# Optimization experiments

Measured on AMD Instinct MI355X. Metric: run time of the kernel, lower is better.

## Reference

```python
import jax, jax.numpy as jnp
import numpy as np
import math

B, SEQ, H, HKV, D = 2, 2048, 32, 8, 128
BLOCK, LOCAL_BLOCKS, VERT_STRIDE = 64, 16, 8
NB = SEQ // BLOCK


def _build_layout():
    # local + vertical-strided causal block-sparse layout (homo heads),
    # converted from CSR to a padded [NB, max_nnz] column-index table.
    q_idx = np.arange(NB)[:, None]
    k_idx = np.arange(NB)[None, :]
    dense = (k_idx <= q_idx) & ((q_idx - k_idx < LOCAL_BLOCKS) | ((k_idx + 1) % VERT_STRIDE == 0))
    max_nnz = int(dense.sum(1).max())  # == 18 for NB=32, local=16, stride=8
    cols = np.zeros((NB, max_nnz), np.int32)
    valid = np.zeros((NB, max_nnz), np.bool_)
    for i in range(NB):
        c = np.nonzero(dense[i])[0]
        cols[i, :c.size] = c
        valid[i, :c.size] = True
    return jnp.asarray(cols), jnp.asarray(valid)


def setup_inputs() -> dict:
    key = jax.random.key(0)
    kq, kk, kv = jax.random.split(key, 3)
    q = jax.random.normal(kq, (B, SEQ, H, D), jnp.float32)
    k = jax.random.normal(kk, (B, SEQ, HKV, D), jnp.float32)
    v = jax.random.normal(kv, (B, SEQ, HKV, D), jnp.float32)
    layout_cols, layout_mask = _build_layout()
    return {"q": q, "k": k, "v": v, "layout_cols": layout_cols, "layout_mask": layout_mask}


def _attn(q, k, v, layout_cols, layout_mask):
    Bn, S, Hq, Dh = q.shape
    Hkv = k.shape[2]
    g = Hq // Hkv               # GQA group size (q_k_ratio)
    nb, nnz = layout_cols.shape
    blk = S // nb               # block_size
    sm_scale = 1.0 / math.sqrt(Dh)
    # reshape to blocks; keep KV at Hkv heads (no repeat) and group q heads
    qb = q.reshape(Bn, nb, blk, Hkv, g, Dh).transpose(0, 3, 4, 1, 2, 5)  # [B,Hkv,g,nb,blk,D]
    kb = k.reshape(Bn, nb, blk, Hkv, Dh).transpose(0, 3, 1, 2, 4)        # [B,Hkv,nb,blk,D]
    vb = v.reshape(Bn, nb, blk, Hkv, Dh).transpose(0, 3, 1, 2, 4)
    # gather only the attended K/V blocks per query block (honors block sparsity)
    kg = jnp.take(kb, layout_cols, axis=2)  # [B,Hkv,nb,nnz,blk,D]
    vg = jnp.take(vb, layout_cols, axis=2)
    scores = jnp.einsum('bhgqmd,bhqknd->bhgqmkn', qb, kg) * sm_scale  # [B,Hkv,g,nb,blk,nnz,blk]
    # token-level causal mask + padded-column mask (past_len = 0 for prefill)
    q_tok = jnp.arange(nb)[:, None] * blk + jnp.arange(blk)[None, :]            # [nb,blk]
    k_tok = layout_cols[:, :, None] * blk + jnp.arange(blk)[None, None, :]      # [nb,nnz,blk]
    valid = layout_mask[:, None, :, None] & (k_tok[:, None] <= q_tok[:, :, None, None])  # [nb,blk,nnz,blk]
    scores = jnp.where(valid[None, None, None], scores, -jnp.inf)
    p = jax.nn.softmax(scores.reshape(Bn, Hkv, g, nb, blk, nnz * blk), axis=-1).reshape(scores.shape)
    out = jnp.einsum('bhgqmkn,bhqknd->bhgqmd', p, vg)
    return out.transpose(0, 3, 4, 1, 2, 5).reshape(Bn, S, Hq, Dh)


def reference(q, k, v, layout_cols, layout_mask):
    return _attn(q, k, v, layout_cols, layout_mask)
```

## Files before the change

kernel.cpp:

```cpp
#include <hip/hip_runtime.h>

#define B_    2
#define SEQ_  2048
#define H_    32
#define HKV_  8
#define D_    128
#define BLK_  64
#define NB_   32
#define LOCAL_ 16
#define VERT_  8

#define PSTR 72
#define NTASK 512
#define NBLOCK 256

typedef __attribute__((ext_vector_type(8))) short bf16x8;
typedef __attribute__((ext_vector_type(4))) float f32x4;

__device__ __forceinline__ unsigned short f2bf(float f) {
    union { float f; unsigned u; } x; x.f = f;
    unsigned u = x.u;
    return (unsigned short)((u + 0x7FFFu + ((u >> 16) & 1u)) >> 16);
}

__device__ __forceinline__ unsigned pk2(float a, float b) {
#if defined(__has_builtin) && __has_builtin(__builtin_amdgcn_cvt_pk_bf16_f32)
    typedef __attribute__((ext_vector_type(2))) __bf16 bf2;
    bf2 r = __builtin_amdgcn_cvt_pk_bf16_f32(a, b);
    unsigned u; __builtin_memcpy(&u, &r, 4); return u;
#else
    return (unsigned)f2bf(a) | ((unsigned)f2bf(b) << 16);
#endif
}

__device__ __forceinline__ int next_valid(int qb, int j) {
    for (++j; j <= qb; ++j)
        if (((qb - j) < LOCAL_) || (((j + 1) & (VERT_ - 1)) == 0)) return j;
    return qb + 1;
}

__device__ __forceinline__ void dma16(const unsigned short* g, unsigned short* l) {
    __builtin_amdgcn_global_load_lds(
        (const __attribute__((address_space(1))) unsigned int*)g,
        (__attribute__((address_space(3))) unsigned int*)l, 16, 0, 0);
}

__global__ __launch_bounds__(256)
void prepass_kernel(const float* __restrict__ kg, const float* __restrict__ vg,
                    unsigned short* __restrict__ Kws, unsigned short* __restrict__ Vws) {
    __shared__ unsigned short Vt[D_ * 72];
    const int bid = blockIdx.x;
    const int b   = bid >> 8;
    const int hkv = (bid >> 5) & 7;
    const int jb  = bid & 31;
    const int tid = threadIdx.x;
    const int rs  = HKV_ * D_;

    const float* kbase = kg + ((size_t)(b * SEQ_ + jb * BLK_) * HKV_ + hkv) * D_;
    const float* vbase = vg + ((size_t)(b * SEQ_ + jb * BLK_) * HKV_ + hkv) * D_;
    unsigned short* Kdst = Kws + ((size_t)(b * 8 + hkv) * SEQ_ + jb * BLK_) * D_;
    unsigned short* Vdst = Vws + ((size_t)(b * 8 + hkv) * NB_ + jb) * (D_ * BLK_);

#pragma unroll
    for (int t = 0; t < 4; ++t) {
        const int q = t * 256 + tid;
        const int row = q >> 4, c = q & 15;
        const float* p = kbase + (size_t)row * rs + c * 8;
        const float4 a = *(const float4*)p;
        const float4 d4 = *(const float4*)(p + 4);
        uint4 u = { pk2(a.x, a.y), pk2(a.z, a.w), pk2(d4.x, d4.y), pk2(d4.z, d4.w) };
        *(uint4*)&Kdst[row * 128 + ((c ^ (row & 15)) << 3)] = u;
    }
#pragma unroll
    for (int t = 0; t < 8; ++t) {
        const int q = t * 256 + tid;
        const int pos = q >> 5, c4 = q & 31;
        const float4 v4 = *(const float4*)(vbase + (size_t)pos * rs + c4 * 4);
        const unsigned u0 = pk2(v4.x, v4.y), u1 = pk2(v4.z, v4.w);
        Vt[(c4 * 4 + 0) * 72 + pos] = (unsigned short)u0;
        Vt[(c4 * 4 + 1) * 72 + pos] = (unsigned short)(u0 >> 16);
        Vt[(c4 * 4 + 2) * 72 + pos] = (unsigned short)u1;
        Vt[(c4 * 4 + 3) * 72 + pos] = (unsigned short)(u1 >> 16);
    }
    __syncthreads();
#pragma unroll
    for (int t = 0; t < 4; ++t) {
        const int q = t * 256 + tid;
        const int d = q >> 3, c = q & 7;
        const uint2 q0 = *(const uint2*)&Vt[d * 72 + c * 8];
        const uint2 q1 = *(const uint2*)&Vt[d * 72 + c * 8 + 4];
        uint4 u = { q0.x, q0.y, q1.x, q1.y };
        *(uint4*)&Vdst[d * 64 + ((c ^ (d & 7)) << 3)] = u;
    }
}

__global__ __launch_bounds__(1024)
void sparse_attn_v2(const float* __restrict__ qg, float* __restrict__ outg,
                    const unsigned short* __restrict__ Kws,
                    const unsigned short* __restrict__ Vws,
                    unsigned* __restrict__ ctr) {
    __shared__ __align__(16) unsigned short Kb[2][BLK_ * D_];
    __shared__ __align__(16) unsigned short Vb[2][D_ * BLK_];
    __shared__ __align__(16) unsigned short Plds[16 * 16 * PSTR];
    __shared__ unsigned taskLds;

    const int tid  = threadIdx.x;
    const int wave = tid >> 6;
    const int lane = tid & 63;
    const int l15  = lane & 15;
    const int quad = lane >> 4;
    const int hsub = wave >> 2;
    const int rt   = wave & 3;

    int csk[4], csv[2];
#pragma unroll
    for (int s = 0; s < 4; ++s)  csk[s] = ((4 * s + quad) ^ l15) << 3;
#pragma unroll
    for (int s = 0; s < 2; ++s)  csv[s] = ((4 * s + quad) ^ (l15 & 7)) << 3;

    const float c2 = 0.12751649736230723f;
    const short oneb = (short)0x3F80;
    const bf16x8 ones = {oneb, oneb, oneb, oneb, oneb, oneb, oneb, oneb};
    unsigned short* pl = &Plds[wave * 16 * PSTR];

    for (;;) {
        __syncthreads();
        if (tid == 0) taskLds = atomicAdd(ctr, 1u);
        __syncthreads();
        const unsigned t = taskLds;
        if (t >= NTASK) break;

        const int qb  = 31 - (int)(t >> 4);
        const int bh  = (int)(t & 15);
        const int b   = bh >> 3;
        const int hkv = bh & 7;
        const int head = hkv * 4 + hsub;

        const unsigned short* Kbh = Kws + (size_t)(b * 8 + hkv) * SEQ_ * D_;
        const unsigned short* Vbh = Vws + (size_t)(b * 8 + hkv) * NB_ * (D_ * BLK_);

        int j = next_valid(qb, -1);
        dma16(Kbh + (size_t)j * (BLK_ * D_) + tid * 8, &Kb[0][wave * 512]);
        dma16(Vbh + (size_t)j * (D_ * BLK_) + tid * 8, &Vb[0][wave * 512]);

        bf16x8 qf[4];
        {
            const int row = qb * BLK_ + rt * 16 + l15;
            const float* qp = qg + ((size_t)(b * SEQ_ + row) * H_ + head) * D_;
#pragma unroll
            for (int s = 0; s < 4; ++s) {
                const float4 a = *(const float4*)(qp + s * 32 + quad * 8);
                const float4 c = *(const float4*)(qp + s * 32 + quad * 8 + 4);
                uint4 u = { pk2(a.x, a.y), pk2(a.z, a.w), pk2(c.x, c.y), pk2(c.z, c.w) };
                __builtin_memcpy(&qf[s], &u, 16);
            }
        }

        f32x4 lacc = f32x4{0.f, 0.f, 0.f, 0.f};
        f32x4 o_acc[8];
#pragma unroll
        for (int t8 = 0; t8 < 8; ++t8) o_acc[t8] = f32x4{0.f, 0.f, 0.f, 0.f};

        __syncthreads();
        int it = 0;
        while (j <= qb) {
            const int jn = next_valid(qb, j);
            const int cur = it & 1;
            if (jn <= qb) {
                dma16(Kbh + (size_t)jn * (BLK_ * D_) + tid * 8, &Kb[cur ^ 1][wave * 512]);
                dma16(Vbh + (size_t)jn * (D_ * BLK_) + tid * 8, &Vb[cur ^ 1][wave * 512]);
            }

            const unsigned short* kb = Kb[cur];
            f32x4 sacc[4];
#pragma unroll
            for (int t4 = 0; t4 < 4; ++t4) {
                f32x4 acc = f32x4{0.f, 0.f, 0.f, 0.f};
                const unsigned short* krow = kb + (t4 * 16 + l15) * 128;
#pragma unroll
                for (int s = 0; s < 4; ++s) {
                    const bf16x8 kf = *(const bf16x8*)(krow + csk[s]);
                    acc = __builtin_amdgcn_mfma_f32_16x16x32_bf16(qf[s], kf, acc, 0, 0, 0);
                }
                sacc[t4] = acc;
            }

            if (j == qb) {
                const int rowbase = rt * 16 + quad * 4;
#pragma unroll
                for (int t4 = 0; t4 < 4; ++t4) {
                    const int col = t4 * 16 + l15;
#pragma unroll
                    for (int r = 0; r < 4; ++r)
                        if (col > rowbase + r) sacc[t4][r] = -INFINITY;
                }
            }

#pragma unroll
            for (int t4 = 0; t4 < 4; ++t4) {
                const float p0 = exp2f(sacc[t4][0] * c2);
                const float p1 = exp2f(sacc[t4][1] * c2);
                const float p2 = exp2f(sacc[t4][2] * c2);
                const float p3 = exp2f(sacc[t4][3] * c2);
                const unsigned u01 = pk2(p0, p1), u23 = pk2(p2, p3);
                const int cb = t4 * 16 + l15;
                pl[(quad * 4 + 0) * PSTR + cb] = (unsigned short)u01;
                pl[(quad * 4 + 1) * PSTR + cb] = (unsigned short)(u01 >> 16);
                pl[(quad * 4 + 2) * PSTR + cb] = (unsigned short)u23;
                pl[(quad * 4 + 3) * PSTR + cb] = (unsigned short)(u23 >> 16);
            }

            const unsigned short* vb = Vb[cur];
#pragma unroll
            for (int s2 = 0; s2 < 2; ++s2) {
                const bf16x8 pf = *(const bf16x8*)&pl[l15 * PSTR + s2 * 32 + quad * 8];
                lacc = __builtin_amdgcn_mfma_f32_16x16x32_bf16(pf, ones, lacc, 0, 0, 0);
#pragma unroll
                for (int t8 = 0; t8 < 8; ++t8) {
                    const bf16x8 vf = *(const bf16x8*)(vb + (t8 * 16 + l15) * 64 + csv[s2]);
                    o_acc[t8] = __builtin_amdgcn_mfma_f32_16x16x32_bf16(pf, vf, o_acc[t8], 0, 0, 0);
                }
            }

            __syncthreads();
            j = jn; ++it;
        }

        const int orow = qb * BLK_ + rt * 16 + quad * 4;
#pragma unroll
        for (int r = 0; r < 4; ++r) {
            const float inv_l = 1.0f / lacc[r];
            float* op = outg + ((size_t)(b * SEQ_ + orow + r) * H_ + head) * D_;
#pragma unroll
            for (int t8 = 0; t8 < 8; ++t8)
                op[t8 * 16 + l15] = o_acc[t8][r] * inv_l;
        }
    }
}

#define KSTR 136
#define VSTR 72
__global__ __launch_bounds__(1024)
void sparse_attn_v1(const float* __restrict__ qg, const float* __restrict__ kg,
                    const float* __restrict__ vg, float* __restrict__ outg,
                    unsigned* __restrict__ ctr) {
    __shared__ __align__(16) unsigned short Klds[BLK_ * KSTR];
    __shared__ __align__(16) unsigned short Vlds[D_ * VSTR];
    __shared__ __align__(16) unsigned short Plds[16 * 16 * PSTR];
    __shared__ unsigned taskLds;

    const int tid  = threadIdx.x;
    const int wave = tid >> 6;
    const int lane = tid & 63;
    const int l15  = lane & 15;
    const int quad = lane >> 4;
    const int hsub = wave >> 2;
    const int rt   = wave & 3;

    const int srow0 = tid >> 5, srow1 = srow0 + 32;
    const int sc4   = tid & 31;
    const int kld0  = srow0 * KSTR + sc4 * 4, kld1 = srow1 * KSTR + sc4 * 4;
    const int vd    = sc4 * 4;
    const int vskew = (sc4 & 7) << 3;
    const int vp0   = (srow0 + vskew) & 63, vp1 = (srow1 + vskew) & 63;
    const size_t stoff0 = (size_t)srow0 * (HKV_ * D_) + sc4 * 4;
    const size_t stoff1 = (size_t)srow1 * (HKV_ * D_) + sc4 * 4;

    const float c2 = 0.12751649736230723f;
    const short oneb = (short)0x3F80;
    const bf16x8 ones = {oneb, oneb, oneb, oneb, oneb, oneb, oneb, oneb};
    unsigned short* pl = &Plds[wave * 16 * PSTR];

    for (;;) {
        __syncthreads();
        if (tid == 0) taskLds = atomicAdd(ctr, 1u);
        __syncthreads();
        const unsigned t = taskLds;
        if (t >= NTASK) break;
        const int qb  = 31 - (int)(t >> 4);
        const int bh  = (int)(t & 15);
        const int b   = bh >> 3;
        const int hkv = bh & 7;
        const int head = hkv * 4 + hsub;
        const float* kbase = kg + ((size_t)(b * SEQ_) * HKV_ + hkv) * D_;
        const float* vbase = vg + ((size_t)(b * SEQ_) * HKV_ + hkv) * D_;
        bf16x8 qf[4];
        {
            const int row = qb * BLK_ + rt * 16 + l15;
            const float* qp = qg + ((size_t)(b * SEQ_ + row) * H_ + head) * D_;
#pragma unroll
            for (int s = 0; s < 4; ++s) {
                const float4 a = *(const float4*)(qp + s * 32 + quad * 8);
                const float4 c = *(const float4*)(qp + s * 32 + quad * 8 + 4);
                uint4 u = { pk2(a.x, a.y), pk2(a.z, a.w), pk2(c.x, c.y), pk2(c.z, c.w) };
                __builtin_memcpy(&qf[s], &u, 16);
            }
        }
        f32x4 lacc = f32x4{0.f, 0.f, 0.f, 0.f};
        f32x4 o_acc[8];
#pragma unroll
        for (int t8 = 0; t8 < 8; ++t8) o_acc[t8] = f32x4{0.f, 0.f, 0.f, 0.f};
        int j = next_valid(qb, -1);
        float4 kpr0, kpr1, vpr0, vpr1;
        {
            const float* kp = kbase + (size_t)j * BLK_ * HKV_ * D_;
            const float* vp = vbase + (size_t)j * BLK_ * HKV_ * D_;
            kpr0 = *(const float4*)(kp + stoff0); kpr1 = *(const float4*)(kp + stoff1);
            vpr0 = *(const float4*)(vp + stoff0); vpr1 = *(const float4*)(vp + stoff1);
        }
        while (j <= qb) {
            const int jn = next_valid(qb, j);
            __syncthreads();
            {
                uint2 u0 = { pk2(kpr0.x, kpr0.y), pk2(kpr0.z, kpr0.w) };
                uint2 u1 = { pk2(kpr1.x, kpr1.y), pk2(kpr1.z, kpr1.w) };
                *(uint2*)&Klds[kld0] = u0;
                *(uint2*)&Klds[kld1] = u1;
                unsigned a0 = pk2(vpr0.x, vpr0.y), a1 = pk2(vpr0.z, vpr0.w);
                Vlds[(vd + 0) * VSTR + vp0] = (unsigned short)a0;
                Vlds[(vd + 1) * VSTR + vp0] = (unsigned short)(a0 >> 16);
                Vlds[(vd + 2) * VSTR + vp0] = (unsigned short)a1;
                Vlds[(vd + 3) * VSTR + vp0] = (unsigned short)(a1 >> 16);
                unsigned b0 = pk2(vpr1.x, vpr1.y), b1 = pk2(vpr1.z, vpr1.w);
                Vlds[(vd + 0) * VSTR + vp1] = (unsigned short)b0;
                Vlds[(vd + 1) * VSTR + vp1] = (unsigned short)(b0 >> 16);
                Vlds[(vd + 2) * VSTR + vp1] = (unsigned short)b1;
                Vlds[(vd + 3) * VSTR + vp1] = (unsigned short)(b1 >> 16);
            }
            __syncthreads();
            if (jn <= qb) {
                const float* kp = kbase + (size_t)jn * BLK_ * HKV_ * D_;
                const float* vp = vbase + (size_t)jn * BLK_ * HKV_ * D_;
                kpr0 = *(const float4*)(kp + stoff0); kpr1 = *(const float4*)(kp + stoff1);
                vpr0 = *(const float4*)(vp + stoff0); vpr1 = *(const float4*)(vp + stoff1);
            }
            f32x4 sacc[4];
#pragma unroll
            for (int t4 = 0; t4 < 4; ++t4) {
                f32x4 acc = f32x4{0.f, 0.f, 0.f, 0.f};
#pragma unroll
                for (int s = 0; s < 4; ++s) {
                    const bf16x8 kf = *(const bf16x8*)&Klds[(t4 * 16 + l15) * KSTR + s * 32 + quad * 8];
                    acc = __builtin_amdgcn_mfma_f32_16x16x32_bf16(qf[s], kf, acc, 0, 0, 0);
                }
                sacc[t4] = acc;
            }
            if (j == qb) {
                const int rowbase = rt * 16 + quad * 4;
#pragma unroll
                for (int t4 = 0; t4 < 4; ++t4) {
                    const int col = t4 * 16 + l15;
#pragma unroll
                    for (int r = 0; r < 4; ++r)
                        if (col > rowbase + r) sacc[t4][r] = -INFINITY;
                }
            }
#pragma unroll
            for (int t4 = 0; t4 < 4; ++t4) {
                const float p0 = exp2f(sacc[t4][0] * c2);
                const float p1 = exp2f(sacc[t4][1] * c2);
                const float p2 = exp2f(sacc[t4][2] * c2);
                const float p3 = exp2f(sacc[t4][3] * c2);
                const unsigned u01 = pk2(p0, p1), u23 = pk2(p2, p3);
                const int cb = t4 * 16 + l15;
                pl[(quad * 4 + 0) * PSTR + cb] = (unsigned short)u01;
                pl[(quad * 4 + 1) * PSTR + cb] = (unsigned short)(u01 >> 16);
                pl[(quad * 4 + 2) * PSTR + cb] = (unsigned short)u23;
                pl[(quad * 4 + 3) * PSTR + cb] = (unsigned short)(u23 >> 16);
            }
#pragma unroll
            for (int s2 = 0; s2 < 2; ++s2) {
                const bf16x8 pf = *(const bf16x8*)&pl[l15 * PSTR + s2 * 32 + quad * 8];
                lacc = __builtin_amdgcn_mfma_f32_16x16x32_bf16(pf, ones, lacc, 0, 0, 0);
                const int k0 = s2 * 32 + quad * 8;
#pragma unroll
                for (int t8 = 0; t8 < 8; ++t8) {
                    const int n  = t8 * 16 + l15;
                    const int p2 = (k0 + (((n >> 2) & 7) << 3)) & 63;
                    const bf16x8 vf = *(const bf16x8*)&Vlds[n * VSTR + p2];
                    o_acc[t8] = __builtin_amdgcn_mfma_f32_16x16x32_bf16(pf, vf, o_acc[t8], 0, 0, 0);
                }
            }
            j = jn;
        }
        const int orow = qb * BLK_ + rt * 16 + quad * 4;
#pragma unroll
        for (int r = 0; r < 4; ++r) {
            const float inv_l = 1.0f / lacc[r];
            float* op = outg + ((size_t)(b * SEQ_ + orow + r) * H_ + head) * D_;
#pragma unroll
            for (int t8 = 0; t8 < 8; ++t8)
                op[t8 * 16 + l15] = o_acc[t8][r] * inv_l;
        }
    }
}

extern "C" void kernel_launch(void* const* d_in, const int* in_sizes, int n_in,
                              void* d_out, int out_size, void* d_ws, size_t ws_size,
                              hipStream_t stream) {
    const float* q = (const float*)d_in[0];
    const float* k = (const float*)d_in[1];
    const float* v = (const float*)d_in[2];
    float* out = (float*)d_out;

    const size_t kws_elems = (size_t)B_ * HKV_ * SEQ_ * D_;
    const size_t need = 256 + 2 * kws_elems * sizeof(unsigned short);
    if (ws_size >= need) {
        unsigned short* Kws = (unsigned short*)((char*)d_ws + 256);
        unsigned short* Vws = Kws + kws_elems;
        hipMemsetAsync(d_ws, 0, 256, stream);
        prepass_kernel<<<dim3(B_ * HKV_ * NB_), dim3(256), 0, stream>>>(k, v, Kws, Vws);
        sparse_attn_v2<<<dim3(NBLOCK), dim3(1024), 0, stream>>>(q, out, Kws, Vws, (unsigned*)d_ws);
    } else {
        hipMemsetAsync(d_ws, 0, sizeof(unsigned), stream);
        sparse_attn_v1<<<dim3(NBLOCK), dim3(1024), 0, stream>>>(q, k, v, out, (unsigned*)d_ws);
    }
}
```

Baseline: 226.8 us.

## Switch attention kernel to 32x32 MFMA with register-resident P via permlane swap

Rewrites the main sparse attention kernel to use 32x32x16 bf16 MFMA tiles instead of 16x16x32. The S=K·Q^T result is computed transposed so the P matrix can be repacked in registers with permlane32_swap, which removes the LDS round-trip for P. Blocks shrink to 512 threads with two blocks per CU, each wave handling 32 query rows. The upper K half of the diagonal tile is skipped for the first row tile. The cost is more registers per wave from the 16-wide accumulators, and the row/lane mapping is more intricate.

```diff
diff --git a/kernel.cpp b/kernel.cpp
--- a/kernel.cpp
+++ b/kernel.cpp
@@ -16,6 +16,7 @@
 
 typedef __attribute__((ext_vector_type(8))) short bf16x8;
 typedef __attribute__((ext_vector_type(4))) float f32x4;
+typedef __attribute__((ext_vector_type(16))) float f32x16;
 
 __device__ __forceinline__ unsigned short f2bf(float f) {
     union { float f; unsigned u; } x; x.f = f;
@@ -31,6 +32,22 @@
 #else
     return (unsigned)f2bf(a) | ((unsigned)f2bf(b) << 16);
 #endif
+}
+
+__device__ __forceinline__ void pswap(unsigned &a, unsigned &b) {
+#if defined(__has_builtin) && __has_builtin(__builtin_amdgcn_permlane32_swap)
+    auto r = __builtin_amdgcn_permlane32_swap((int)a, (int)b, false, false);
+    a = (unsigned)r[0]; b = (unsigned)r[1];
+#else
+    asm("v_permlane32_swap_b32 %0, %1" : "+v"(a), "+v"(b));
+#endif
+}
+
+__device__ __forceinline__ f32x16 zero16() {
+    f32x16 z;
+#pragma unroll
+    for (int i = 0; i < 16; ++i) z[i] = 0.f;
+    return z;
 }
 
 __device__ __forceinline__ int next_valid(int qb, int j) {
@@ -94,34 +111,33 @@
     }
 }
 
-__global__ __launch_bounds__(1024)
-void sparse_attn_v2(const float* __restrict__ qg, float* __restrict__ outg,
+__global__ __launch_bounds__(512, 2)
+void sparse_attn_v3(const float* __restrict__ qg, float* __restrict__ outg,
                     const unsigned short* __restrict__ Kws,
                     const unsigned short* __restrict__ Vws,
                     unsigned* __restrict__ ctr) {
     __shared__ __align__(16) unsigned short Kb[2][BLK_ * D_];
     __shared__ __align__(16) unsigned short Vb[2][D_ * BLK_];
-    __shared__ __align__(16) unsigned short Plds[16 * 16 * PSTR];
     __shared__ unsigned taskLds;
 
     const int tid  = threadIdx.x;
     const int wave = tid >> 6;
     const int lane = tid & 63;
-    const int l15  = lane & 15;
-    const int quad = lane >> 4;
-    const int hsub = wave >> 2;
-    const int rt   = wave & 3;
-
-    int csk[4], csv[2];
-#pragma unroll
-    for (int s = 0; s < 4; ++s)  csk[s] = ((4 * s + quad) ^ l15) << 3;
-#pragma unroll
-    for (int s = 0; s < 2; ++s)  csv[s] = ((4 * s + quad) ^ (l15 & 7)) << 3;
+    const int q5   = lane & 31;
+    const int h    = lane >> 5;
+    const int hsub = wave >> 1;
+    const int rt2  = wave & 1;
+
+    int cskA[8];
+#pragma unroll
+    for (int dk = 0; dk < 8; ++dk) cskA[dk] = ((((dk * 2) | h) ^ (lane & 15)) << 3);
+    int csvB[4];
+#pragma unroll
+    for (int kc = 0; kc < 4; ++kc) csvB[kc] = ((((kc * 2) | h) ^ (lane & 7)) << 3);
 
     const float c2 = 0.12751649736230723f;
     const short oneb = (short)0x3F80;
     const bf16x8 ones = {oneb, oneb, oneb, oneb, oneb, oneb, oneb, oneb};
-    unsigned short* pl = &Plds[wave * 16 * PSTR];
 
     for (;;) {
         __syncthreads();
@@ -140,26 +156,32 @@
         const unsigned short* Vbh = Vws + (size_t)(b * 8 + hkv) * NB_ * (D_ * BLK_);
 
         int j = next_valid(qb, -1);
-        dma16(Kbh + (size_t)j * (BLK_ * D_) + tid * 8, &Kb[0][wave * 512]);
-        dma16(Vbh + (size_t)j * (D_ * BLK_) + tid * 8, &Vb[0][wave * 512]);
-
-        bf16x8 qf[4];
         {
-            const int row = qb * BLK_ + rt * 16 + l15;
-            const float* qp = qg + ((size_t)(b * SEQ_ + row) * H_ + head) * D_;
-#pragma unroll
-            for (int s = 0; s < 4; ++s) {
-                const float4 a = *(const float4*)(qp + s * 32 + quad * 8);
-                const float4 c = *(const float4*)(qp + s * 32 + quad * 8 + 4);
+            const size_t off = (size_t)j * (BLK_ * D_);
+#pragma unroll
+            for (int i = 0; i < 2; ++i) {
+                dma16(Kbh + off + i * 4096 + tid * 8, &Kb[0][i * 4096 + wave * 512]);
+                dma16(Vbh + off + i * 4096 + tid * 8, &Vb[0][i * 4096 + wave * 512]);
+            }
+        }
+
+        bf16x8 qf[8];
+        {
+            const int row = qb * BLK_ + rt2 * 32 + q5;
+            const float* qp = qg + ((size_t)(b * SEQ_ + row) * H_ + head) * D_ + h * 8;
+#pragma unroll
+            for (int dk = 0; dk < 8; ++dk) {
+                const float4 a = *(const float4*)(qp + dk * 16);
+                const float4 c = *(const float4*)(qp + dk * 16 + 4);
                 uint4 u = { pk2(a.x, a.y), pk2(a.z, a.w), pk2(c.x, c.y), pk2(c.z, c.w) };
-                __builtin_memcpy(&qf[s], &u, 16);
-            }
-        }
-
-        f32x4 lacc = f32x4{0.f, 0.f, 0.f, 0.f};
-        f32x4 o_acc[8];
-#pragma unroll
-        for (int t8 = 0; t8 < 8; ++t8) o_acc[t8] = f32x4{0.f, 0.f, 0.f, 0.f};
+                __builtin_memcpy(&qf[dk], &u, 16);
+            }
+        }
+
+        f32x16 lacc = zero16();
+        f32x16 o_acc[4];
+#pragma unroll
+        for (int dt = 0; dt < 4; ++dt) o_acc[dt] = zero16();
 
         __syncthreads();
         int it = 0;
@@ -167,58 +189,85 @@
             const int jn = next_valid(qb, j);
             const int cur = it & 1;
             if (jn <= qb) {
-                dma16(Kbh + (size_t)jn * (BLK_ * D_) + tid * 8, &Kb[cur ^ 1][wave * 512]);
-                dma16(Vbh + (size_t)jn * (D_ * BLK_) + tid * 8, &Vb[cur ^ 1][wave * 512]);
-            }
+                const size_t off = (size_t)jn * (BLK_ * D_);
+#pragma unroll
+                for (int i = 0; i < 2; ++i) {
+                    dma16(Kbh + off + i * 4096 + tid * 8, &Kb[cur ^ 1][i * 4096 + wave * 512]);
+                    dma16(Vbh + off + i * 4096 + tid * 8, &Vb[cur ^ 1][i * 4096 + wave * 512]);
+                }
+            }
+
+            const bool diag  = (j == qb);
+            const bool diagw = diag && (rt2 == 0);
 
             const unsigned short* kb = Kb[cur];
-            f32x4 sacc[4];
-#pragma unroll
-            for (int t4 = 0; t4 < 4; ++t4) {
-                f32x4 acc = f32x4{0.f, 0.f, 0.f, 0.f};
-                const unsigned short* krow = kb + (t4 * 16 + l15) * 128;
-#pragma unroll
-                for (int s = 0; s < 4; ++s) {
-                    const bf16x8 kf = *(const bf16x8*)(krow + csk[s]);
-                    acc = __builtin_amdgcn_mfma_f32_16x16x32_bf16(qf[s], kf, acc, 0, 0, 0);
-                }
-                sacc[t4] = acc;
-            }
-
-            if (j == qb) {
-                const int rowbase = rt * 16 + quad * 4;
-#pragma unroll
-                for (int t4 = 0; t4 < 4; ++t4) {
-                    const int col = t4 * 16 + l15;
-#pragma unroll
-                    for (int r = 0; r < 4; ++r)
-                        if (col > rowbase + r) sacc[t4][r] = -INFINITY;
-                }
-            }
-
-#pragma unroll
-            for (int t4 = 0; t4 < 4; ++t4) {
-                const float p0 = exp2f(sacc[t4][0] * c2);
-                const float p1 = exp2f(sacc[t4][1] * c2);
-                const float p2 = exp2f(sacc[t4][2] * c2);
-                const float p3 = exp2f(sacc[t4][3] * c2);
-                const unsigned u01 = pk2(p0, p1), u23 = pk2(p2, p3);
-                const int cb = t4 * 16 + l15;
-                pl[(quad * 4 + 0) * PSTR + cb] = (unsigned short)u01;
-                pl[(quad * 4 + 1) * PSTR + cb] = (unsigned short)(u01 >> 16);
-                pl[(quad * 4 + 2) * PSTR + cb] = (unsigned short)u23;
-                pl[(quad * 4 + 3) * PSTR + cb] = (unsigned short)(u23 >> 16);
+            f32x16 s0 = zero16(), s1 = zero16();
+            {
+                const unsigned short* k0r = kb + q5 * 128;
+                const unsigned short* k1r = kb + (32 + q5) * 128;
+#pragma unroll
+                for (int dk = 0; dk < 8; ++dk) {
+                    const bf16x8 kf0 = *(const bf16x8*)(k0r + cskA[dk]);
+                    s0 = __builtin_amdgcn_mfma_f32_32x32x16_bf16(kf0, qf[dk], s0, 0, 0, 0);
+                }
+                if (!diagw) {
+#pragma unroll
+                    for (int dk = 0; dk < 8; ++dk) {
+                        const bf16x8 kf1 = *(const bf16x8*)(k1r + cskA[dk]);
+                        s1 = __builtin_amdgcn_mfma_f32_32x32x16_bf16(kf1, qf[dk], s1, 0, 0, 0);
+                    }
+                }
+            }
+
+            if (diag) {
+                if (rt2 == 0) {
+#pragma unroll
+                    for (int r = 0; r < 16; ++r) {
+                        const int crow = (r & 3) + 8 * (r >> 2) + 4 * h;
+                        if (crow > q5) s0[r] = -INFINITY;
+                    }
+                } else {
+#pragma unroll
+                    for (int r = 0; r < 16; ++r) {
+                        const int crow = (r & 3) + 8 * (r >> 2) + 4 * h;
+                        if (crow > q5) s1[r] = -INFINITY;
+                    }
+                }
+            }
+
+#pragma unroll
+            for (int r = 0; r < 16; ++r) s0[r] = exp2f(s0[r] * c2);
+            if (!diagw) {
+#pragma unroll
+                for (int r = 0; r < 16; ++r) s1[r] = exp2f(s1[r] * c2);
+            }
+
+            bf16x8 pa[4];
+#pragma unroll
+            for (int kc = 0; kc < 4; ++kc) {
+                if (kc >= 2 && diagw) continue;
+                const f32x16 &pp = (kc >= 2) ? s1 : s0;
+                const int b0 = (kc & 1) * 8;
+                unsigned A0 = pk2(pp[b0 + 0], pp[b0 + 1]);
+                unsigned B0 = pk2(pp[b0 + 4], pp[b0 + 5]);
+                unsigned A1 = pk2(pp[b0 + 2], pp[b0 + 3]);
+                unsigned B1 = pk2(pp[b0 + 6], pp[b0 + 7]);
+                pswap(A0, B0);
+                pswap(A1, B1);
+                uint4 u = { A0, A1, B0, B1 };
+                __builtin_memcpy(&pa[kc], &u, 16);
+                lacc = __builtin_amdgcn_mfma_f32_32x32x16_bf16(pa[kc], ones, lacc, 0, 0, 0);
             }
 
             const unsigned short* vb = Vb[cur];
 #pragma unroll
-            for (int s2 = 0; s2 < 2; ++s2) {
-                const bf16x8 pf = *(const bf16x8*)&pl[l15 * PSTR + s2 * 32 + quad * 8];
-                lacc = __builtin_amdgcn_mfma_f32_16x16x32_bf16(pf, ones, lacc, 0, 0, 0);
-#pragma unroll
-                for (int t8 = 0; t8 < 8; ++t8) {
-                    const bf16x8 vf = *(const bf16x8*)(vb + (t8 * 16 + l15) * 64 + csv[s2]);
-                    o_acc[t8] = __builtin_amdgcn_mfma_f32_16x16x32_bf16(pf, vf, o_acc[t8], 0, 0, 0);
+            for (int dt = 0; dt < 4; ++dt) {
+                const unsigned short* vrow = vb + (dt * 32 + q5) * 64;
+#pragma unroll
+                for (int kc = 0; kc < 4; ++kc) {
+                    if (kc >= 2 && diagw) continue;
+                    const bf16x8 vf = *(const bf16x8*)(vrow + csvB[kc]);
+                    o_acc[dt] = __builtin_amdgcn_mfma_f32_32x32x16_bf16(pa[kc], vf, o_acc[dt], 0, 0, 0);
                 }
             }
 
@@ -226,14 +275,16 @@
             j = jn; ++it;
         }
 
-        const int orow = qb * BLK_ + rt * 16 + quad * 4;
-#pragma unroll
-        for (int r = 0; r < 4; ++r) {
-            const float inv_l = 1.0f / lacc[r];
-            float* op = outg + ((size_t)(b * SEQ_ + orow + r) * H_ + head) * D_;
-#pragma unroll
-            for (int t8 = 0; t8 < 8; ++t8)
-                op[t8 * 16 + l15] = o_acc[t8][r] * inv_l;
+        const int rowbase = qb * BLK_ + rt2 * 32;
+#pragma unroll
+        for (int r = 0; r < 16; ++r) {
+            const int row = rowbase + (r & 3) + 8 * (r >> 2) + 4 * h;
+            const float inv = 1.0f / lacc[r];
+            float* op = outg + ((size_t)(b * SEQ_ + row) * H_ + head) * D_ + q5;
+            op[0]  = o_acc[0][r] * inv;
+            op[32] = o_acc[1][r] * inv;
+            op[64] = o_acc[2][r] * inv;
+            op[96] = o_acc[3][r] * inv;
         }
     }
 }
@@ -410,7 +461,7 @@
         unsigned short* Vws = Kws + kws_elems;
         hipMemsetAsync(d_ws, 0, 256, stream);
         prepass_kernel<<<dim3(B_ * HKV_ * NB_), dim3(256), 0, stream>>>(k, v, Kws, Vws);
-        sparse_attn_v2<<<dim3(NBLOCK), dim3(1024), 0, stream>>>(q, out, Kws, Vws, (unsigned*)d_ws);
+        sparse_attn_v3<<<dim3(NBLOCK), dim3(512), 0, stream>>>(q, out, Kws, Vws, (unsigned*)d_ws);
     } else {
         hipMemsetAsync(d_ws, 0, sizeof(unsigned), stream);
         sparse_attn_v1<<<dim3(NBLOCK), dim3(1024), 0, stream>>>(q, k, v, out, (unsigned*)d_ws);
```

Result: slower. 239.8 us (+5.7%).

## Pre-swizzle V into MFMA fragment order and read V directly from global

Applied to the files above, without the earlier changes.

The prepass now writes V in exact per-lane MFMA B-fragment order, so the attention kernel loads each V fragment straight from global/L2 with one 16-byte read instead of DMA-staging V blocks through double-buffered LDS. This removes the V LDS buffers and their DMA traffic, which halves LDS use and may allow more overlap. The cost is exposed global-load latency inside the PV loop, with no prefetch. Separately, the task counter reset moves from a memset into the prepass kernel, dropping one launch.

```diff
diff --git a/kernel.cpp b/kernel.cpp
--- a/kernel.cpp
+++ b/kernel.cpp
@@ -47,7 +47,8 @@
 
 __global__ __launch_bounds__(256)
 void prepass_kernel(const float* __restrict__ kg, const float* __restrict__ vg,
-                    unsigned short* __restrict__ Kws, unsigned short* __restrict__ Vws) {
+                    unsigned short* __restrict__ Kws, unsigned short* __restrict__ Vws,
+                    unsigned* __restrict__ ctr) {
     __shared__ unsigned short Vt[D_ * 72];
     const int bid = blockIdx.x;
     const int b   = bid >> 8;
@@ -55,6 +56,8 @@
     const int jb  = bid & 31;
     const int tid = threadIdx.x;
     const int rs  = HKV_ * D_;
+
+    if (bid == 0 && tid == 0) *ctr = 0;
 
     const float* kbase = kg + ((size_t)(b * SEQ_ + jb * BLK_) * HKV_ + hkv) * D_;
     const float* vbase = vg + ((size_t)(b * SEQ_ + jb * BLK_) * HKV_ + hkv) * D_;
@@ -85,22 +88,23 @@
     __syncthreads();
 #pragma unroll
     for (int t = 0; t < 4; ++t) {
-        const int q = t * 256 + tid;
-        const int d = q >> 3, c = q & 7;
-        const uint2 q0 = *(const uint2*)&Vt[d * 72 + c * 8];
-        const uint2 q1 = *(const uint2*)&Vt[d * 72 + c * 8 + 4];
+        const int cv  = t * 256 + tid;
+        const int l15 = cv & 15, quad = (cv >> 4) & 3, s2 = (cv >> 6) & 1, t8 = (cv >> 7) & 7;
+        const int d    = t8 * 16 + l15;
+        const int pos0 = s2 * 32 + quad * 8;
+        const uint2 q0 = *(const uint2*)&Vt[d * 72 + pos0];
+        const uint2 q1 = *(const uint2*)&Vt[d * 72 + pos0 + 4];
         uint4 u = { q0.x, q0.y, q1.x, q1.y };
-        *(uint4*)&Vdst[d * 64 + ((c ^ (d & 7)) << 3)] = u;
+        *(uint4*)&Vdst[cv * 8] = u;
     }
 }
 
 __global__ __launch_bounds__(1024)
-void sparse_attn_v2(const float* __restrict__ qg, float* __restrict__ outg,
-                    const unsigned short* __restrict__ Kws,
-                    const unsigned short* __restrict__ Vws,
-                    unsigned* __restrict__ ctr) {
+void sparse_attn_v10(const float* __restrict__ qg, float* __restrict__ outg,
+                     const unsigned short* __restrict__ Kws,
+                     const unsigned short* __restrict__ Vws,
+                     unsigned* __restrict__ ctr) {
     __shared__ __align__(16) unsigned short Kb[2][BLK_ * D_];
-    __shared__ __align__(16) unsigned short Vb[2][D_ * BLK_];
     __shared__ __align__(16) unsigned short Plds[16 * 16 * PSTR];
     __shared__ unsigned taskLds;
 
@@ -112,11 +116,9 @@
     const int hsub = wave >> 2;
     const int rt   = wave & 3;
 
-    int csk[4], csv[2];
+    int csk[4];
 #pragma unroll
     for (int s = 0; s < 4; ++s)  csk[s] = ((4 * s + quad) ^ l15) << 3;
-#pragma unroll
-    for (int s = 0; s < 2; ++s)  csv[s] = ((4 * s + quad) ^ (l15 & 7)) << 3;
 
     const float c2 = 0.12751649736230723f;
     const short oneb = (short)0x3F80;
@@ -138,10 +140,10 @@
 
         const unsigned short* Kbh = Kws + (size_t)(b * 8 + hkv) * SEQ_ * D_;
         const unsigned short* Vbh = Vws + (size_t)(b * 8 + hkv) * NB_ * (D_ * BLK_);
+        const unsigned short* Vln = Vbh + lane * 8;
 
         int j = next_valid(qb, -1);
         dma16(Kbh + (size_t)j * (BLK_ * D_) + tid * 8, &Kb[0][wave * 512]);
-        dma16(Vbh + (size_t)j * (D_ * BLK_) + tid * 8, &Vb[0][wave * 512]);
 
         bf16x8 qf[4];
         {
@@ -166,10 +168,8 @@
         while (j <= qb) {
             const int jn = next_valid(qb, j);
             const int cur = it & 1;
-            if (jn <= qb) {
+            if (jn <= qb)
                 dma16(Kbh + (size_t)jn * (BLK_ * D_) + tid * 8, &Kb[cur ^ 1][wave * 512]);
-                dma16(Vbh + (size_t)jn * (D_ * BLK_) + tid * 8, &Vb[cur ^ 1][wave * 512]);
-            }
 
             const unsigned short* kb = Kb[cur];
             f32x4 sacc[4];
@@ -210,14 +210,14 @@
                 pl[(quad * 4 + 3) * PSTR + cb] = (unsigned short)(u23 >> 16);
             }
 
-            const unsigned short* vb = Vb[cur];
+            const unsigned short* vj = Vln + (size_t)j * (D_ * BLK_);
 #pragma unroll
             for (int s2 = 0; s2 < 2; ++s2) {
                 const bf16x8 pf = *(const bf16x8*)&pl[l15 * PSTR + s2 * 32 + quad * 8];
                 lacc = __builtin_amdgcn_mfma_f32_16x16x32_bf16(pf, ones, lacc, 0, 0, 0);
 #pragma unroll
                 for (int t8 = 0; t8 < 8; ++t8) {
-                    const bf16x8 vf = *(const bf16x8*)(vb + (t8 * 16 + l15) * 64 + csv[s2]);
+                    const bf16x8 vf = *(const bf16x8*)(vj + (t8 * 2 + s2) * 512);
                     o_acc[t8] = __builtin_amdgcn_mfma_f32_16x16x32_bf16(pf, vf, o_acc[t8], 0, 0, 0);
                 }
             }
@@ -408,9 +408,8 @@
     if (ws_size >= need) {
         unsigned short* Kws = (unsigned short*)((char*)d_ws + 256);
         unsigned short* Vws = Kws + kws_elems;
-        hipMemsetAsync(d_ws, 0, 256, stream);
-        prepass_kernel<<<dim3(B_ * HKV_ * NB_), dim3(256), 0, stream>>>(k, v, Kws, Vws);
-        sparse_attn_v2<<<dim3(NBLOCK), dim3(1024), 0, stream>>>(q, out, Kws, Vws, (unsigned*)d_ws);
+        prepass_kernel<<<dim3(B_ * HKV_ * NB_), dim3(256), 0, stream>>>(k, v, Kws, Vws, (unsigned*)d_ws);
+        sparse_attn_v10<<<dim3(NBLOCK), dim3(1024), 0, stream>>>(q, out, Kws, Vws, (unsigned*)d_ws);
     } else {
         hipMemsetAsync(d_ws, 0, sizeof(unsigned), stream);
         sparse_attn_v1<<<dim3(NBLOCK), dim3(1024), 0, stream>>>(q, k, v, out, (unsigned*)d_ws);
```

Measured after the change: 278.2 us. 22.7% more time.
